# Optimization experiments

Hardware: AMD Instinct MI355X
Metric: run time of the kernel (lower is better)

The kernel has to match this reference:

```python
import jax, jax.numpy as jnp
import numpy as np

# Fano plane lines: for each line (i, j, k) we combine colonies i and j and write to k.
FANO_LINES = np.array([(0, 1, 2), (0, 3, 4), (0, 5, 6), (1, 3, 5), (4, 1, 6), (3, 2, 6), (4, 2, 5)], dtype=np.int32)

B, C, Z = 131072, 7, 64  # batch, colonies (fixed 7), z_dim


def setup_inputs() -> dict:
    key = jax.random.key(0)
    k1, k2, k3 = jax.random.split(key, 3)
    colony_states = jax.random.normal(k1, (B, C, Z), dtype=jnp.float32)
    # nn.Linear(2*z_dim, z_dim): weight [Z, 2Z], bias [Z]
    lim = 1.0 / np.sqrt(2 * Z)
    W = jax.random.uniform(k2, (Z, 2 * Z), dtype=jnp.float32, minval=-lim, maxval=lim)
    b = jax.random.uniform(k3, (Z,), dtype=jnp.float32, minval=-lim, maxval=lim)
    gates = jnp.ones((7,), dtype=jnp.float32) / 7.0  # nn.Parameter init
    return {"colony_states": colony_states, "W": W, "b": b, "gates": gates}


def reference(colony_states, W, b, gates):
    I = jnp.asarray(FANO_LINES[:, 0])
    J = jnp.asarray(FANO_LINES[:, 1])
    K = jnpp = jnp.asarray(FANO_LINES[:, 2])
    g = jax.nn.softmax(gates)  # [7]
    # Vectorized gather over all 7 lines at once: [B, 7, 2Z]
    combined = jnp.concatenate([colony_states[:, I], colony_states[:, J]], axis=-1)
    # Shared linear applied to every line: [B, 7, Z]
    delta = jnp.einsum('blf,zf->blz', combined, W) + b
    gated = g[None, :, None] * delta
    # Gated scatter-add into target colonies; K has duplicates, .add accumulates.
    deltas = jnp.zeros_like(colony_states).at[:, K].add(gated)
    return colony_states + deltas
```

## Files before the change

kernel.cpp:

```cpp
#include <hip/hip_runtime.h>
#include <math.h>


using bf16x8  = __attribute__((ext_vector_type(8))) __bf16;
using floatx4 = __attribute__((ext_vector_type(4))) float;

#define BATCHES 16
#define DSTR    516

__constant__ int c_nl[7]    = {0,0,1,0,1,2,3};
__constant__ int c_us[7][3] = {{0,0,0},{0,0,0},{0,0,0},{0,0,0},{0,0,0},{1,3,0},{0,3,2}};
__constant__ int c_vs[7][3] = {{0,0,0},{0,0,0},{4,0,0},{0,0,0},{6,0,0},{6,5,0},{7,4,5}};
__constant__ int c_g [7][3] = {{0,0,0},{0,0,0},{0,0,0},{0,0,0},{1,0,0},{3,6,0},{2,4,5}};
__constant__ int wv_cA[4] = {0,1,3,4};
__constant__ int wv_cB[4] = {2,1,3,5};
__constant__ int wv_sA[4] = {0,1,2,3};
__constant__ int wv_sB[4] = {5,4,6,7};

__device__ __forceinline__ __bf16 tobf(float f) {
    unsigned u = __builtin_bit_cast(unsigned, f);
    u = (u + 0x7FFFu + ((u >> 16) & 1u)) >> 16;
    unsigned short s = (unsigned short)u;
    return __builtin_bit_cast(__bf16, s);
}
__device__ __forceinline__ bf16x8 cvt8(floatx4 a, floatx4 b) {
    bf16x8 r;
    r[0]=tobf(a[0]); r[1]=tobf(a[1]); r[2]=tobf(a[2]); r[3]=tobf(a[3]);
    r[4]=tobf(b[0]); r[5]=tobf(b[1]); r[6]=tobf(b[2]); r[7]=tobf(b[3]);
    return r;
}

__global__ __launch_bounds__(256, 3)
void fano_kernel(const float* __restrict__ S,
                 const float* __restrict__ W,
                 const float* __restrict__ bias,
                 const float* __restrict__ gates,
                 float* __restrict__ out, int nt)
{
    __shared__ float Dlds[BATCHES * DSTR];
    __shared__ unsigned char Wb[128 * 128];
    __shared__ float Blds[64];
    __shared__ float gsm[8];

    const int tid  = threadIdx.x;
    const int lane = tid & 63;
    const int wave = tid >> 6;
    const int nl   = lane & 15;
    const int qg   = lane >> 4;

    const int cA = wv_cA[wave], cB = wv_cB[wave];
    const int sA = wv_sA[wave], sB = wv_sB[wave];
    const bool dup = (cA == cB);

    long long tile = blockIdx.x;
    floatx4 aA[4], aB[4];
    {
        const float* p = S + ((long long)tile * BATCHES + nl) * 448 + cA * 64 + qg * 8;
        aA[0] = *(const floatx4*)p;      aA[1] = *(const floatx4*)(p + 4);
        aA[2] = *(const floatx4*)(p + 32); aA[3] = *(const floatx4*)(p + 36);
        if (!dup) {
            const float* q = S + ((long long)tile * BATCHES + nl) * 448 + cB * 64 + qg * 8;
            aB[0] = *(const floatx4*)q;      aB[1] = *(const floatx4*)(q + 4);
            aB[2] = *(const floatx4*)(q + 32); aB[3] = *(const floatx4*)(q + 36);
        }
    }

    for (int idx = tid; idx < 1024; idx += 256) {
        const int n = idx >> 3, u = idx & 7;
        const float* src = (n < 64) ? (W + n * 128 + u * 8)
                                    : (W + (n - 64) * 128 + 64 + u * 8);
        floatx4 w0 = *(const floatx4*)src;
        floatx4 w1 = *(const floatx4*)(src + 4);
        bf16x8 v = cvt8(w0, w1);
        *(bf16x8*)(Wb + n * 128 + ((u ^ (n & 7)) << 4)) = v;
    }
    if (tid < 64) Blds[tid] = bias[tid];
    if (tid < 7) {
        float mx = gates[0];
        #pragma unroll
        for (int i = 1; i < 7; ++i) mx = fmaxf(mx, gates[i]);
        float se = 0.f, ev = 0.f;
        #pragma unroll
        for (int i = 0; i < 7; ++i) {
            float e = __expf(gates[i] - mx);
            se += e;
            if (i == tid) ev = e;
        }
        gsm[tid] = ev / se;
    }
    __syncthreads();

    const int swz0 = ((qg)     ^ (nl & 7)) << 4;
    const int swz1 = ((4 + qg) ^ (nl & 7)) << 4;

    for (;;) {
        const long long next = tile + gridDim.x;

        bf16x8 afA0 = cvt8(aA[0], aA[1]);
        bf16x8 afA1 = cvt8(aA[2], aA[3]);
        bf16x8 afB0 = dup ? afA0 : cvt8(aB[0], aB[1]);
        bf16x8 afB1 = dup ? afA1 : cvt8(aB[2], aB[3]);

        floatx4 accA[4], accB[4];
        #pragma unroll
        for (int t = 0; t < 4; ++t) {
            accA[t] = (floatx4){0.f,0.f,0.f,0.f};
            accB[t] = (floatx4){0.f,0.f,0.f,0.f};
        }
        #pragma unroll
        for (int t = 0; t < 4; ++t) {
            const unsigned char* r0 = Wb + (t * 16 + nl) * 128;
            const unsigned char* r1 = Wb + ((t + 4) * 16 + nl) * 128;
            accA[t] = __builtin_amdgcn_mfma_f32_16x16x32_bf16(afA0, *(const bf16x8*)(r0 + swz0), accA[t], 0,0,0);
            accA[t] = __builtin_amdgcn_mfma_f32_16x16x32_bf16(afA1, *(const bf16x8*)(r0 + swz1), accA[t], 0,0,0);
            accB[t] = __builtin_amdgcn_mfma_f32_16x16x32_bf16(afB0, *(const bf16x8*)(r1 + swz0), accB[t], 0,0,0);
            accB[t] = __builtin_amdgcn_mfma_f32_16x16x32_bf16(afB1, *(const bf16x8*)(r1 + swz1), accB[t], 0,0,0);
        }
        #pragma unroll
        for (int t = 0; t < 4; ++t)
            #pragma unroll
            for (int r = 0; r < 4; ++r) {
                Dlds[(qg * 4 + r) * DSTR + sA * 64 + t * 16 + nl] = accA[t][r];
                Dlds[(qg * 4 + r) * DSTR + sB * 64 + t * 16 + nl] = accB[t][r];
            }
        __syncthreads();

        const bool more = (next < (long long)nt);
        if (more) {
            const float* p = S + (next * BATCHES + nl) * 448 + cA * 64 + qg * 8;
            aA[0] = *(const floatx4*)p;      aA[1] = *(const floatx4*)(p + 4);
            aA[2] = *(const floatx4*)(p + 32); aA[3] = *(const floatx4*)(p + 36);
            if (!dup) {
                const float* q = S + (next * BATCHES + nl) * 448 + cB * 64 + qg * 8;
                aB[0] = *(const floatx4*)q;      aB[1] = *(const floatx4*)(q + 4);
                aB[2] = *(const floatx4*)(q + 32); aB[3] = *(const floatx4*)(q + 36);
            }
        }

        const long long obase = tile * (BATCHES * 7 * 64);
        #pragma unroll
        for (int it = 0; it < 7; ++it) {
            const int u   = it * 256 + tid;
            const int row = u >> 4;
            const int q   = u & 15;
            const int b   = row / 7;
            const int c   = row - b * 7;
            floatx4 o  = *(const floatx4*)(S + obase + u * 4);
            floatx4 bq = *(const floatx4*)(Blds + q * 4);
            const float* dbase = Dlds + b * DSTR + q * 4;
            const int n = c_nl[c];
            for (int e = 0; e < n; ++e) {
                const float g = gsm[c_g[c][e]];
                floatx4 uu = *(const floatx4*)(dbase + c_us[c][e] * 64);
                floatx4 vv = *(const floatx4*)(dbase + c_vs[c][e] * 64);
                o += g * (uu + vv + bq);
            }
            *(floatx4*)(out + obase + u * 4) = o;
        }
        __syncthreads();
        if (!more) break;
        tile = next;
    }
}

extern "C" void kernel_launch(void* const* d_in, const int* in_sizes, int n_in,
                              void* d_out, int out_size, void* d_ws, size_t ws_size,
                              hipStream_t stream) {
    const float* S     = (const float*)d_in[0];
    const float* W     = (const float*)d_in[1];
    const float* bias  = (const float*)d_in[2];
    const float* gates = (const float*)d_in[3];
    float* out = (float*)d_out;

    const int B  = in_sizes[0] / (7 * 64);
    const int nt = B / BATCHES;
    int grid = 768;
    if (grid > nt) grid = nt;
    fano_kernel<<<grid, 256, 0, stream>>>(S, W, bias, gates, out, nt);
}
```

Baseline: 443.2 us.

## Restructure Fano kernel so each wave owns whole tiles with register epilogue

```diff
diff --git a/kernel.cpp b/kernel.cpp
--- a/kernel.cpp
+++ b/kernel.cpp
@@ -5,42 +5,23 @@
 using bf16x8  = __attribute__((ext_vector_type(8))) __bf16;
 using floatx4 = __attribute__((ext_vector_type(4))) float;
 
-#define BATCHES 16
-#define DSTR    516
+#define TPW 4
 
-__constant__ int c_nl[7]    = {0,0,1,0,1,2,3};
-__constant__ int c_us[7][3] = {{0,0,0},{0,0,0},{0,0,0},{0,0,0},{0,0,0},{1,3,0},{0,3,2}};
-__constant__ int c_vs[7][3] = {{0,0,0},{0,0,0},{4,0,0},{0,0,0},{6,0,0},{6,5,0},{7,4,5}};
-__constant__ int c_g [7][3] = {{0,0,0},{0,0,0},{0,0,0},{0,0,0},{1,0,0},{3,6,0},{2,4,5}};
-__constant__ int wv_cA[4] = {0,1,3,4};
-__constant__ int wv_cB[4] = {2,1,3,5};
-__constant__ int wv_sA[4] = {0,1,2,3};
-__constant__ int wv_sB[4] = {5,4,6,7};
-
-__device__ __forceinline__ __bf16 tobf(float f) {
-    unsigned u = __builtin_bit_cast(unsigned, f);
-    u = (u + 0x7FFFu + ((u >> 16) & 1u)) >> 16;
-    unsigned short s = (unsigned short)u;
-    return __builtin_bit_cast(__bf16, s);
-}
 __device__ __forceinline__ bf16x8 cvt8(floatx4 a, floatx4 b) {
     bf16x8 r;
-    r[0]=tobf(a[0]); r[1]=tobf(a[1]); r[2]=tobf(a[2]); r[3]=tobf(a[3]);
-    r[4]=tobf(b[0]); r[5]=tobf(b[1]); r[6]=tobf(b[2]); r[7]=tobf(b[3]);
+    r[0]=(__bf16)a[0]; r[1]=(__bf16)a[1]; r[2]=(__bf16)a[2]; r[3]=(__bf16)a[3];
+    r[4]=(__bf16)b[0]; r[5]=(__bf16)b[1]; r[6]=(__bf16)b[2]; r[7]=(__bf16)b[3];
     return r;
 }
 
-__global__ __launch_bounds__(256, 3)
+__global__ __launch_bounds__(256, 2)
 void fano_kernel(const float* __restrict__ S,
                  const float* __restrict__ W,
                  const float* __restrict__ bias,
                  const float* __restrict__ gates,
                  float* __restrict__ out, int nt)
 {
-    __shared__ float Dlds[BATCHES * DSTR];
-    __shared__ unsigned char Wb[128 * 128];
-    __shared__ float Blds[64];
-    __shared__ float gsm[8];
+    __shared__ __align__(16) unsigned char Wb[64 * 256];
 
     const int tid  = threadIdx.x;
     const int lane = tid & 63;
@@ -48,118 +29,133 @@
     const int nl   = lane & 15;
     const int qg   = lane >> 4;
 
-    const int cA = wv_cA[wave], cB = wv_cB[wave];
-    const int sA = wv_sA[wave], sB = wv_sB[wave];
-    const bool dup = (cA == cB);
-
-    long long tile = blockIdx.x;
-    floatx4 aA[4], aB[4];
-    {
-        const float* p = S + ((long long)tile * BATCHES + nl) * 448 + cA * 64 + qg * 8;
-        aA[0] = *(const floatx4*)p;      aA[1] = *(const floatx4*)(p + 4);
-        aA[2] = *(const floatx4*)(p + 32); aA[3] = *(const floatx4*)(p + 36);
-        if (!dup) {
-            const float* q = S + ((long long)tile * BATCHES + nl) * 448 + cB * 64 + qg * 8;
-            aB[0] = *(const floatx4*)q;      aB[1] = *(const floatx4*)(q + 4);
-            aB[2] = *(const floatx4*)(q + 32); aB[3] = *(const floatx4*)(q + 36);
-        }
+    #pragma unroll
+    for (int k = 0; k < 4; ++k) {
+        const int idx = tid + k * 256;
+        const int z = idx >> 4, u = idx & 15;
+        const float* src = W + z * 128 + u * 8;
+        bf16x8 v = cvt8(*(const floatx4*)src, *(const floatx4*)(src + 4));
+        *(bf16x8*)(Wb + z * 256 + ((u ^ (z & 15)) << 4)) = v;
     }
 
-    for (int idx = tid; idx < 1024; idx += 256) {
-        const int n = idx >> 3, u = idx & 7;
-        const float* src = (n < 64) ? (W + n * 128 + u * 8)
-                                    : (W + (n - 64) * 128 + 64 + u * 8);
-        floatx4 w0 = *(const floatx4*)src;
-        floatx4 w1 = *(const floatx4*)(src + 4);
-        bf16x8 v = cvt8(w0, w1);
-        *(bf16x8*)(Wb + n * 128 + ((u ^ (n & 7)) << 4)) = v;
-    }
-    if (tid < 64) Blds[tid] = bias[tid];
-    if (tid < 7) {
+    float g[7];
+    {
         float mx = gates[0];
         #pragma unroll
         for (int i = 1; i < 7; ++i) mx = fmaxf(mx, gates[i]);
-        float se = 0.f, ev = 0.f;
+        float se = 0.f;
         #pragma unroll
-        for (int i = 0; i < 7; ++i) {
-            float e = __expf(gates[i] - mx);
-            se += e;
-            if (i == tid) ev = e;
-        }
-        gsm[tid] = ev / se;
+        for (int i = 0; i < 7; ++i) { g[i] = __expf(gates[i] - mx); se += g[i]; }
+        const float inv = 1.f / se;
+        #pragma unroll
+        for (int i = 0; i < 7; ++i) g[i] *= inv;
     }
+
+    floatx4 bv[4];
+    #pragma unroll
+    for (int t = 0; t < 4; ++t) bv[t] = *(const floatx4*)(bias + t * 16 + qg * 4);
+
     __syncthreads();
 
-    const int swz0 = ((qg)     ^ (nl & 7)) << 4;
-    const int swz1 = ((4 + qg) ^ (nl & 7)) << 4;
+    const int wid = blockIdx.x * 4 + wave;
 
-    for (;;) {
-        const long long next = tile + gridDim.x;
+    for (int i = 0; i < TPW; ++i) {
+        const int tile = wid * TPW + i;
+        if (tile >= nt) break;
 
-        bf16x8 afA0 = cvt8(aA[0], aA[1]);
-        bf16x8 afA1 = cvt8(aA[2], aA[3]);
-        bf16x8 afB0 = dup ? afA0 : cvt8(aB[0], aB[1]);
-        bf16x8 afB1 = dup ? afA1 : cvt8(aB[2], aB[3]);
+        const long long rb = ((long long)tile * 16 + nl) * 448;
+        const float* srow = S + rb;
+        float*       orow = out + rb;
 
-        floatx4 accA[4], accB[4];
+        floatx4 tmp[6][4];
         #pragma unroll
-        for (int t = 0; t < 4; ++t) {
-            accA[t] = (floatx4){0.f,0.f,0.f,0.f};
-            accB[t] = (floatx4){0.f,0.f,0.f,0.f};
+        for (int c = 0; c < 6; ++c) {
+            const float* p = srow + c * 64 + qg * 8;
+            tmp[c][0] = *(const floatx4*)p;
+            tmp[c][1] = *(const floatx4*)(p + 4);
+            tmp[c][2] = *(const floatx4*)(p + 32);
+            tmp[c][3] = *(const floatx4*)(p + 36);
         }
+        floatx4 cp[3][4];
         #pragma unroll
-        for (int t = 0; t < 4; ++t) {
-            const unsigned char* r0 = Wb + (t * 16 + nl) * 128;
-            const unsigned char* r1 = Wb + ((t + 4) * 16 + nl) * 128;
-            accA[t] = __builtin_amdgcn_mfma_f32_16x16x32_bf16(afA0, *(const bf16x8*)(r0 + swz0), accA[t], 0,0,0);
-            accA[t] = __builtin_amdgcn_mfma_f32_16x16x32_bf16(afA1, *(const bf16x8*)(r0 + swz1), accA[t], 0,0,0);
-            accB[t] = __builtin_amdgcn_mfma_f32_16x16x32_bf16(afB0, *(const bf16x8*)(r1 + swz0), accB[t], 0,0,0);
-            accB[t] = __builtin_amdgcn_mfma_f32_16x16x32_bf16(afB1, *(const bf16x8*)(r1 + swz1), accB[t], 0,0,0);
+        for (int j = 0; j < 3; ++j) {
+            const int c = (j == 2) ? 3 : j;
+            #pragma unroll
+            for (int t = 0; t < 4; ++t)
+                cp[j][t] = *(const floatx4*)(srow + c * 64 + t * 16 + qg * 4);
         }
+
+        bf16x8 sb[6][2];
         #pragma unroll
-        for (int t = 0; t < 4; ++t)
+        for (int c = 0; c < 6; ++c) {
+            sb[c][0] = cvt8(tmp[c][0], tmp[c][1]);
+            sb[c][1] = cvt8(tmp[c][2], tmp[c][3]);
+        }
+
+        #pragma unroll
+        for (int j = 0; j < 3; ++j) {
+            const int c = (j == 2) ? 3 : j;
             #pragma unroll
-            for (int r = 0; r < 4; ++r) {
-                Dlds[(qg * 4 + r) * DSTR + sA * 64 + t * 16 + nl] = accA[t][r];
-                Dlds[(qg * 4 + r) * DSTR + sB * 64 + t * 16 + nl] = accB[t][r];
+            for (int t = 0; t < 4; ++t)
+                *(floatx4*)(orow + c * 64 + t * 16 + qg * 4) = cp[j][t];
+        }
+
+        floatx4 res[4][4];
+        #pragma unroll
+        for (int j = 0; j < 4; ++j) {
+            const int c = (j == 0) ? 2 : (j == 1) ? 4 : (j == 2) ? 5 : 6;
+            #pragma unroll
+            for (int t = 0; t < 4; ++t)
+                res[j][t] = *(const floatx4*)(srow + c * 64 + t * 16 + qg * 4);
+        }
+
+        #pragma unroll
+        for (int hb = 0; hb < 2; ++hb) {
+            floatx4 acc[8][2];
+            #pragma unroll
+            for (int s8 = 0; s8 < 8; ++s8) {
+                acc[s8][0] = (floatx4){0.f,0.f,0.f,0.f};
+                acc[s8][1] = (floatx4){0.f,0.f,0.f,0.f};
             }
-        __syncthreads();
-
-        const bool more = (next < (long long)nt);
-        if (more) {
-            const float* p = S + (next * BATCHES + nl) * 448 + cA * 64 + qg * 8;
-            aA[0] = *(const floatx4*)p;      aA[1] = *(const floatx4*)(p + 4);
-            aA[2] = *(const floatx4*)(p + 32); aA[3] = *(const floatx4*)(p + 36);
-            if (!dup) {
-                const float* q = S + (next * BATCHES + nl) * 448 + cB * 64 + qg * 8;
-                aB[0] = *(const floatx4*)q;      aB[1] = *(const floatx4*)(q + 4);
-                aB[2] = *(const floatx4*)(q + 32); aB[3] = *(const floatx4*)(q + 36);
+            #pragma unroll
+            for (int tp = 0; tp < 2; ++tp) {
+                const int t    = hb * 2 + tp;
+                const int rowb = (t * 16 + nl) * 256;
+                #pragma unroll
+                for (int h = 0; h < 4; ++h) {
+                    const bf16x8 wf =
+                        *(const bf16x8*)(Wb + rowb + (((h * 4 + qg) ^ nl) << 4));
+                    const int kb = h & 1;
+                    if (h < 2) {
+                        acc[0][tp] = __builtin_amdgcn_mfma_f32_16x16x32_bf16(wf, sb[0][kb], acc[0][tp], 0,0,0);
+                        acc[1][tp] = __builtin_amdgcn_mfma_f32_16x16x32_bf16(wf, sb[1][kb], acc[1][tp], 0,0,0);
+                        acc[2][tp] = __builtin_amdgcn_mfma_f32_16x16x32_bf16(wf, sb[3][kb], acc[2][tp], 0,0,0);
+                        acc[3][tp] = __builtin_amdgcn_mfma_f32_16x16x32_bf16(wf, sb[4][kb], acc[3][tp], 0,0,0);
+                    } else {
+                        acc[4][tp] = __builtin_amdgcn_mfma_f32_16x16x32_bf16(wf, sb[1][kb], acc[4][tp], 0,0,0);
+                        acc[5][tp] = __builtin_amdgcn_mfma_f32_16x16x32_bf16(wf, sb[2][kb], acc[5][tp], 0,0,0);
+                        acc[6][tp] = __builtin_amdgcn_mfma_f32_16x16x32_bf16(wf, sb[3][kb], acc[6][tp], 0,0,0);
+                        acc[7][tp] = __builtin_amdgcn_mfma_f32_16x16x32_bf16(wf, sb[5][kb], acc[7][tp], 0,0,0);
+                    }
+                }
+            }
+            #pragma unroll
+            for (int tp = 0; tp < 2; ++tp) {
+                const int t = hb * 2 + tp;
+                const floatx4 b4 = bv[t];
+                floatx4 o2 = res[0][t] + g[0] * (acc[0][tp] + acc[4][tp] + b4);
+                floatx4 o4 = res[1][t] + g[1] * (acc[0][tp] + acc[6][tp] + b4);
+                floatx4 o5 = res[2][t] + g[3] * (acc[1][tp] + acc[6][tp] + b4)
+                                       + g[6] * (acc[3][tp] + acc[5][tp] + b4);
+                floatx4 o6 = res[3][t] + g[2] * (acc[0][tp] + acc[7][tp] + b4)
+                                       + g[4] * (acc[3][tp] + acc[4][tp] + b4)
+                                       + g[5] * (acc[2][tp] + acc[5][tp] + b4);
+                *(floatx4*)(orow + 2 * 64 + t * 16 + qg * 4) = o2;
+                *(floatx4*)(orow + 4 * 64 + t * 16 + qg * 4) = o4;
+                *(floatx4*)(orow + 5 * 64 + t * 16 + qg * 4) = o5;
+                *(floatx4*)(orow + 6 * 64 + t * 16 + qg * 4) = o6;
             }
         }
-
-        const long long obase = tile * (BATCHES * 7 * 64);
-        #pragma unroll
-        for (int it = 0; it < 7; ++it) {
-            const int u   = it * 256 + tid;
-            const int row = u >> 4;
-            const int q   = u & 15;
-            const int b   = row / 7;
-            const int c   = row - b * 7;
-            floatx4 o  = *(const floatx4*)(S + obase + u * 4);
-            floatx4 bq = *(const floatx4*)(Blds + q * 4);
-            const float* dbase = Dlds + b * DSTR + q * 4;
-            const int n = c_nl[c];
-            for (int e = 0; e < n; ++e) {
-                const float g = gsm[c_g[c][e]];
-                floatx4 uu = *(const floatx4*)(dbase + c_us[c][e] * 64);
-                floatx4 vv = *(const floatx4*)(dbase + c_vs[c][e] * 64);
-                o += g * (uu + vv + bq);
-            }
-            *(floatx4*)(out + obase + u * 4) = o;
-        }
-        __syncthreads();
-        if (!more) break;
-        tile = next;
     }
 }
 
@@ -173,8 +169,8 @@
     float* out = (float*)d_out;
 
     const int B  = in_sizes[0] / (7 * 64);
-    const int nt = B / BATCHES;
-    int grid = 768;
-    if (grid > nt) grid = nt;
+    const int nt = B / 16;
+    const int tiles_per_block = 4 * TPW;
+    int grid = (nt + tiles_per_block - 1) / tiles_per_block;
     fano_kernel<<<grid, 256, 0, stream>>>(S, W, bias, gates, out, nt);
 }
```

After: 429.8 us. 1.03x faster.
